# Performance work log

Measured on AMD Instinct MI355X. Metric: run time of the kernel, lower is better.

Reference implementation:

```python
import jax, jax.numpy as jnp
import numpy as np

B, C, H, W = 8, 384, 32, 32
NH, DK, DV = 8, 48, 48
CFF = 4 * C
L = H * W
NBIAS = (2 * H - 1) * (2 * W - 1)
LN_EPS = 1e-5


def _relative_indices(height, width):
    # rel_idx[q, k] = (gy_k - gy_q + H) * W + (gx_k - gx_q + W), matching the torch loop
    gy, gx = np.meshgrid(np.arange(height), np.arange(width), indexing='ij')
    gy = gy.ravel(); gx = gx.ravel()
    rel = (gy[None, :] - gy[:, None] + height) * width + (gx[None, :] - gx[:, None] + width)
    return jnp.asarray(rel, dtype=jnp.int64)


def setup_inputs() -> dict:
    key = jax.random.key(0)
    ks = jax.random.split(key, 10)
    s = 0.02  # small init scale
    return {
        'x': jax.random.normal(ks[0], (B, C, H, W), dtype=jnp.float32),
        'gamma': jnp.ones((C,), jnp.float32),
        'beta': jnp.zeros((C,), jnp.float32),
        'Wq': jax.random.normal(ks[1], (NH * DK, C), jnp.float32) * s,
        'Wk': jax.random.normal(ks[2], (NH * DK, C), jnp.float32) * s,
        'Wv': jax.random.normal(ks[3], (NH * DV, C), jnp.float32) * s,
        'Wo': jax.random.normal(ks[4], (C, NH * DV), jnp.float32) * s,
        'bo': jnp.zeros((C,), jnp.float32),
        'rel_bias': jax.random.normal(ks[5], (NH, NBIAS), jnp.float32),
        'fc1_w': jax.random.normal(ks[6], (CFF, C), jnp.float32) * s,
        'fc1_b': jnp.zeros((CFF,), jnp.float32),
        'fc2_w': jax.random.normal(ks[7], (C, CFF), jnp.float32) * s,
        'fc2_b': jnp.zeros((C,), jnp.float32),
        'rel_idx': _relative_indices(H, W),
    }


def reference(x, gamma, beta, Wq, Wk, Wv, Wo, bo, rel_bias,
              fc1_w, fc1_b, fc2_w, fc2_b, rel_idx):
    b, c, h_sp, w_sp = x.shape
    l = h_sp * w_sp
    nh = rel_bias.shape[0]
    dk = Wq.shape[0] // nh
    dv = Wv.shape[0] // nh

    # LayerNorm over channel dim (NHWC), then flatten to tokens [b, l, c]
    t = jnp.transpose(x, (0, 2, 3, 1))
    mu = jnp.mean(t, axis=-1, keepdims=True)
    var = jnp.mean(jnp.square(t - mu), axis=-1, keepdims=True)
    t = (t - mu) / jnp.sqrt(var + LN_EPS) * gamma + beta
    tok = t.reshape(b, l, c)

    q = (tok @ Wq.T).reshape(b, l, nh, dk)
    k = (tok @ Wk.T).reshape(b, l, nh, dk)
    v = (tok @ Wv.T).reshape(b, l, nh, dv)

    # gathered relative position bias: [nh, l, l]
    bias = rel_bias[:, rel_idx]
    # note: original applies NO 1/sqrt(d_k) scaling
    scores = jnp.einsum('blhd,bmhd->bhlm', q, k) + bias[None]
    attn = jax.nn.softmax(scores, axis=-1)
    out = jnp.einsum('bhlm,bmhd->blhd', attn, v).reshape(b, l, nh * dv)
    out = out @ Wo.T + bo  # [b, l, c]
    out = jnp.transpose(out, (0, 2, 1)).reshape(b, c, h_sp, w_sp)

    y = x + out  # attention residual (x_stem = x, no downsampling)

    # FFN: 1x1 convs == per-pixel linear over channels; exact (erf) gelu as torch default
    u = jnp.einsum('bchw,oc->bohw', y, fc1_w) + fc1_b[None, :, None, None]
    u = jax.nn.gelu(u, approximate=False)
    u = jnp.einsum('bchw,oc->bohw', u, fc2_w) + fc2_b[None, :, None, None]
    return y + u
```

## Files before the change

kernel.cpp:

```cpp
#include <hip/hip_runtime.h>
#include <math.h>

#define SL 1024
#define CH 384
#define NHEAD 8
#define DH 48
#define NBIAS 3969
#define NTOK 8192
#define BATCH 8
#define CFF 1536
#define LN_EPS 1e-5f
#define QKVLD 1152
#define HMS 3145728

#define WQKV_OFF 0
#define WO_OFF   442368
#define F1_OFF   589824
#define F2_OFF   1179648
#define WTOT     1769472

typedef float floatx4 __attribute__((ext_vector_type(4)));
typedef short bf16x8 __attribute__((ext_vector_type(8)));

__device__ __forceinline__ unsigned f2bf_u(float f) {
  unsigned u = __float_as_uint(f);
  return (u + 0x7fffu + ((u >> 16) & 1u)) >> 16;
}
__device__ __forceinline__ unsigned pack2(float a, float b) {
  return f2bf_u(a) | (f2bf_u(b) << 16);
}

__device__ __forceinline__ void gload_lds16(const void* g, void* l) {
  __builtin_amdgcn_global_load_lds(
      (const __attribute__((address_space(1))) void*)g,
      (__attribute__((address_space(3))) void*)l, 16, 0, 0);
}

__global__ void k_w2bf(const float* __restrict__ Wq, const float* __restrict__ Wk,
                       const float* __restrict__ Wv, const float* __restrict__ Wo,
                       const float* __restrict__ f1, const float* __restrict__ f2,
                       short* __restrict__ dst) {
  size_t i = ((size_t)blockIdx.x * 256 + threadIdx.x) * 8;
  if (i >= WTOT) return;
  const float* s;
  size_t base;
  if (i < 147456)        { s = Wq; base = 0; }
  else if (i < 294912)   { s = Wk; base = 147456; }
  else if (i < WO_OFF)   { s = Wv; base = 294912; }
  else if (i < F1_OFF)   { s = Wo; base = WO_OFF; }
  else if (i < F2_OFF)   { s = f1; base = F1_OFF; }
  else                   { s = f2; base = F2_OFF; }
  const float4* p = (const float4*)(s + (i - base));
  float4 a = p[0], b = p[1];
  uint4 o;
  o.x = pack2(a.x, a.y); o.y = pack2(a.z, a.w);
  o.z = pack2(b.x, b.y); o.w = pack2(b.z, b.w);
  *(uint4*)(dst + i) = o;
}

__global__ __launch_bounds__(256) void k_ln_fused(
    const float* __restrict__ x, const float* __restrict__ gamma,
    const float* __restrict__ beta, short* __restrict__ tok) {
  __shared__ float sx[32][385];
  int b = blockIdx.y, l0 = blockIdx.x * 32;
  int tid = threadIdx.x;
  const float* xb = x + (size_t)b * CH * SL;
  int cr = tid >> 3, ls = (tid & 7) * 4;
#pragma unroll
  for (int c0 = 0; c0 < CH; c0 += 32) {
    int c = c0 + cr;
    float4 v = *(const float4*)(xb + (size_t)c * SL + l0 + ls);
    sx[ls + 0][c] = v.x; sx[ls + 1][c] = v.y;
    sx[ls + 2][c] = v.z; sx[ls + 3][c] = v.w;
  }
  __syncthreads();
  int tl = tid >> 3, p = tid & 7;
  float vals[48];
  float s = 0.f, q = 0.f;
#pragma unroll
  for (int i = 0; i < 48; i++) {
    float v = sx[tl][p * 48 + i];
    vals[i] = v; s += v; q += v * v;
  }
  s += __shfl_xor(s, 1, 64); q += __shfl_xor(q, 1, 64);
  s += __shfl_xor(s, 2, 64); q += __shfl_xor(q, 2, 64);
  s += __shfl_xor(s, 4, 64); q += __shfl_xor(q, 4, 64);
  float mu = s * (1.0f / CH);
  float rstd = rsqrtf(q * (1.0f / CH) - mu * mu + LN_EPS);
  short* orow = tok + (size_t)(b * SL + l0 + tl) * CH + p * 48;
#pragma unroll
  for (int i = 0; i < 48; i += 2) {
    float a = (vals[i] - mu) * rstd * gamma[p * 48 + i] + beta[p * 48 + i];
    float c = (vals[i + 1] - mu) * rstd * gamma[p * 48 + i + 1] + beta[p * 48 + i + 1];
    *(unsigned*)(orow + i) = pack2(a, c);
  }
}

template <int BM, bool GELU, bool HAS_BIAS, int RES_MODE, int OUT_MODE>
__global__ __launch_bounds__(256) void k_gemm_mfma(
    const short* __restrict__ A, const short* __restrict__ W,
    const float* __restrict__ bias, const float* __restrict__ res,
    float* __restrict__ Cf, short* __restrict__ Cb, float* __restrict__ Ct,
    short* __restrict__ Chm, int N, int K) {
  constexpr int MI = BM / 32;
  constexpr int ASI = BM * 2 / 64;
  __shared__ short As[BM * 64];
  __shared__ short Bs[128 * 64];
  int tid = threadIdx.x;
  int wid = tid >> 6, lane = tid & 63;
  int lanelo = lane & 15, quad = lane >> 4;
  int wm = wid & 1, wn = wid >> 1;
  int m0 = blockIdx.y * BM, n0 = blockIdx.x * 128;

  const short* Aga[ASI];
  short* Ala[ASI];
#pragma unroll
  for (int s = 0; s < ASI; s++) {
    int p = wid * (BM * 2) + s * 64 + lane;
    int row = p >> 3, ch = (p & 7) ^ (row & 7);
    Aga[s] = A + (size_t)(m0 + row) * K + ch * 8;
    Ala[s] = As + (wid * (BM * 2) + s * 64) * 8;
  }
  const short* Bga[4];
  short* Bla[4];
#pragma unroll
  for (int s = 0; s < 4; s++) {
    int p = wid * 256 + s * 64 + lane;
    int row = p >> 3, ch = (p & 7) ^ (row & 7);
    Bga[s] = W + (size_t)(n0 + row) * K + ch * 8;
    Bla[s] = Bs + (wid * 256 + s * 64) * 8;
  }

  floatx4 acc[MI][4];
#pragma unroll
  for (int i = 0; i < MI; i++)
#pragma unroll
    for (int j = 0; j < 4; j++) acc[i][j] = {0.f, 0.f, 0.f, 0.f};

  int x8 = lanelo & 7;
  int ca0 = (quad ^ x8) * 8;
  int ca1 = ((quad + 4) ^ x8) * 8;

  for (int k0 = 0; k0 < K; k0 += 64) {
    __syncthreads();
#pragma unroll
    for (int s = 0; s < ASI; s++) gload_lds16(Aga[s] + k0, Ala[s]);
#pragma unroll
    for (int s = 0; s < 4; s++) gload_lds16(Bga[s] + k0, Bla[s]);
    __syncthreads();
#pragma unroll
    for (int h = 0; h < 2; h++) {
      int co = h ? ca1 : ca0;
      bf16x8 af[MI], bq[4];
#pragma unroll
      for (int i = 0; i < MI; i++)
        af[i] = *(const bf16x8*)&As[(wm * (BM / 2) + i * 16 + lanelo) * 64 + co];
#pragma unroll
      for (int j = 0; j < 4; j++)
        bq[j] = *(const bf16x8*)&Bs[(wn * 64 + j * 16 + lanelo) * 64 + co];
#pragma unroll
      for (int i = 0; i < MI; i++)
#pragma unroll
        for (int j = 0; j < 4; j++)
          acc[i][j] = __builtin_amdgcn_mfma_f32_16x16x32_bf16(af[i], bq[j], acc[i][j], 0, 0, 0);
    }
  }

  int colb = n0 + wn * 64 + lanelo;
  float bvv[4];
#pragma unroll
  for (int j = 0; j < 4; j++) bvv[j] = HAS_BIAS ? bias[colb + j * 16] : 0.0f;
#pragma unroll
  for (int i = 0; i < MI; i++) {
    int r = m0 + wm * (BM / 2) + i * 16 + quad * 4;
    int bb = r >> 10, ll = r & 1023;
#pragma unroll
    for (int j = 0; j < 4; j++) {
      int c = colb + j * 16;
      float4 rv = {0.f, 0.f, 0.f, 0.f};
      if (RES_MODE == 2) rv = *(const float4*)(res + ((size_t)bb * CH + c) * SL + ll);
      float vv[4];
#pragma unroll
      for (int reg = 0; reg < 4; reg++) {
        float v = acc[i][j][reg] + bvv[j];
        if (RES_MODE == 1) v += res[(size_t)(r + reg) * N + c];
        if (RES_MODE == 2) v += (&rv.x)[reg];
        if (GELU) v = 0.5f * v * (1.0f + erff(v * 0.7071067811865476f));
        vv[reg] = v;
      }
      if (OUT_MODE & 1) {
#pragma unroll
        for (int reg = 0; reg < 4; reg++) Cf[(size_t)(r + reg) * N + c] = vv[reg];
      }
      if (OUT_MODE & 2) {
#pragma unroll
        for (int reg = 0; reg < 4; reg++) Cb[(size_t)(r + reg) * N + c] = (short)f2bf_u(vv[reg]);
      }
      if (OUT_MODE & 4) {
        float4 ov = {vv[0], vv[1], vv[2], vv[3]};
        *(float4*)(Ct + ((size_t)bb * CH + c) * SL + ll) = ov;
      }
      if (OUT_MODE & 8) {
        int part = c / 384;
        int rem = c - part * 384;
        int hh = rem / 48, dd = rem - hh * 48;
        short* dst = Chm + (size_t)part * HMS +
                     ((size_t)(bb * NHEAD + hh) * SL + ll) * 48 + dd;
#pragma unroll
        for (int reg = 0; reg < 4; reg++) dst[reg * 48] = (short)f2bf_u(vv[reg]);
      }
    }
  }
}

__global__ __launch_bounds__(256) void k_attn_mfma(
    const short* __restrict__ qh, const short* __restrict__ kh,
    const short* __restrict__ vh, const float* __restrict__ rel_bias,
    short* __restrict__ ao) {
  __shared__ short QP[128 * 72];
  __shared__ short Ks[64 * 72];
  __shared__ short Vts[48 * 72];

  int b = blockIdx.z, h = blockIdx.y;
  int l0 = blockIdx.x * 128;
  int tid = threadIdx.x;
  int wid = tid >> 6, lane = tid & 63;
  int lanelo = lane & 15, quad = lane >> 4;
  size_t hb = ((size_t)b * NHEAD + h) * SL;
  size_t bSL = (size_t)b * SL;
  const float* rbh = rel_bias + h * NBIAS;
  const short* kbase = kh + hb * 48;
  const short* vbase = vh + hb * 48;

  {
    const short* qsrc = qh + (hb + l0) * 48;
    for (int g = tid; g < 768; g += 256) {
      int row = g / 6, pos = g - row * 6;
      *(uint4*)&QP[row * 72 + pos * 8] = *(const uint4*)(qsrc + g * 8);
    }
  }
  for (int z = tid; z < 128 * 8; z += 256) {
    int r = z >> 3, u = z & 7;
    ((unsigned*)&QP[r * 72 + 48])[u] = 0u;
    if (r < 64) ((unsigned*)&Ks[r * 72 + 48])[u] = 0u;
  }

  int kg = 2 * tid;
  int krow = kg / 6, kpos = kg - krow * 6;
  int vmp = tid & 31, vdg = tid >> 5;

  uint4 kr0, kr1, vr0, vr1;
  if (tid < 192) {
    kr0 = *(const uint4*)(kbase + kg * 8);
    kr1 = *(const uint4*)(kbase + kg * 8 + 8);
    const short* vs = vbase + (2 * vmp) * 48 + vdg * 8;
    vr0 = *(const uint4*)vs;
    vr1 = *(const uint4*)(vs + 48);
  }
  __syncthreads();

  bf16x8 aq[2][2];
#pragma unroll
  for (int i = 0; i < 2; i++) {
    aq[i][0] = *(const bf16x8*)&QP[(wid * 32 + i * 16 + lanelo) * 72 + quad * 8];
    aq[i][1] = *(const bf16x8*)&QP[(wid * 32 + i * 16 + lanelo) * 72 + 32 + quad * 8];
  }

  floatx4 O[2][3];
#pragma unroll
  for (int i = 0; i < 2; i++)
#pragma unroll
    for (int d = 0; d < 3; d++) O[i][d] = {0.f, 0.f, 0.f, 0.f};
  float lsum[2][4] = {{0.f, 0.f, 0.f, 0.f}, {0.f, 0.f, 0.f, 0.f}};
  int boff[2];
#pragma unroll
  for (int i = 0; i < 2; i++)
    boff[i] = 1056 - (l0 + wid * 32 + i * 16 + quad * 4) + lanelo;

  short* Pw = &QP[wid * 32 * 72];

  for (int mt = 0; mt < SL; mt += 64) {
    __syncthreads();
    if (tid < 192) {
      *(uint4*)&Ks[krow * 72 + kpos * 8] = kr0;
      *(uint4*)&Ks[krow * 72 + (kpos + 1) * 8] = kr1;
      union { uint4 u; unsigned short s[8]; } va, vb;
      va.u = vr0; vb.u = vr1;
#pragma unroll
      for (int i = 0; i < 8; i++) {
        unsigned pk = (unsigned)va.s[i] | ((unsigned)vb.s[i] << 16);
        *(unsigned*)&Vts[(vdg * 8 + i) * 72 + 2 * vmp] = pk;
      }
    }
    __syncthreads();
    if (mt + 64 < SL && tid < 192) {
      const short* ks = kbase + (size_t)(mt + 64) * 48;
      kr0 = *(const uint4*)(ks + kg * 8);
      kr1 = *(const uint4*)(ks + kg * 8 + 8);
      const short* vs = vbase + (size_t)(mt + 64 + 2 * vmp) * 48 + vdg * 8;
      vr0 = *(const uint4*)vs;
      vr1 = *(const uint4*)(vs + 48);
    }

    bf16x8 kb[4][2];
#pragma unroll
    for (int nt = 0; nt < 4; nt++) {
      kb[nt][0] = *(const bf16x8*)&Ks[(nt * 16 + lanelo) * 72 + quad * 8];
      kb[nt][1] = *(const bf16x8*)&Ks[(nt * 16 + lanelo) * 72 + 32 + quad * 8];
    }

#pragma unroll
    for (int i = 0; i < 2; i++) {
      floatx4 s[4];
#pragma unroll
      for (int nt = 0; nt < 4; nt++) {
        floatx4 a = {0.f, 0.f, 0.f, 0.f};
        a = __builtin_amdgcn_mfma_f32_16x16x32_bf16(aq[i][0], kb[nt][0], a, 0, 0, 0);
        a = __builtin_amdgcn_mfma_f32_16x16x32_bf16(aq[i][1], kb[nt][1], a, 0, 0, 0);
        s[nt] = a;
      }
#pragma unroll
      for (int nt = 0; nt < 4; nt++) {
        int mo = mt + nt * 16;
#pragma unroll
        for (int reg = 0; reg < 4; reg++) {
          float e = __expf(s[nt][reg] + rbh[boff[i] - reg + mo]);
          lsum[i][reg] += e;
          Pw[(i * 16 + quad * 4 + reg) * 72 + nt * 16 + lanelo] = (short)f2bf_u(e);
        }
      }
    }
    __asm__ volatile("s_waitcnt lgkmcnt(0)" ::: "memory");
    bf16x8 pa[2][2];
#pragma unroll
    for (int i = 0; i < 2; i++) {
      pa[i][0] = *(const bf16x8*)&Pw[(i * 16 + lanelo) * 72 + quad * 8];
      pa[i][1] = *(const bf16x8*)&Pw[(i * 16 + lanelo) * 72 + 32 + quad * 8];
    }
#pragma unroll
    for (int d = 0; d < 3; d++) {
      bf16x8 v0 = *(const bf16x8*)&Vts[(d * 16 + lanelo) * 72 + quad * 8];
      bf16x8 v1 = *(const bf16x8*)&Vts[(d * 16 + lanelo) * 72 + 32 + quad * 8];
#pragma unroll
      for (int i = 0; i < 2; i++) {
        O[i][d] = __builtin_amdgcn_mfma_f32_16x16x32_bf16(pa[i][0], v0, O[i][d], 0, 0, 0);
        O[i][d] = __builtin_amdgcn_mfma_f32_16x16x32_bf16(pa[i][1], v1, O[i][d], 0, 0, 0);
      }
    }
  }

#pragma unroll
  for (int i = 0; i < 2; i++)
#pragma unroll
    for (int reg = 0; reg < 4; reg++) {
      float s = lsum[i][reg];
      s += __shfl_xor(s, 1, 64);
      s += __shfl_xor(s, 2, 64);
      s += __shfl_xor(s, 4, 64);
      s += __shfl_xor(s, 8, 64);
      float inv = 1.0f / s;
      size_t base =
          (bSL + (size_t)(l0 + wid * 32 + i * 16 + quad * 4 + reg)) * CH + h * DH;
      ao[base + 0 + lanelo]  = (short)f2bf_u(O[i][0][reg] * inv);
      ao[base + 16 + lanelo] = (short)f2bf_u(O[i][1][reg] * inv);
      ao[base + 32 + lanelo] = (short)f2bf_u(O[i][2][reg] * inv);
    }
}

extern "C" void kernel_launch(void* const* d_in, const int* in_sizes, int n_in,
                              void* d_out, int out_size, void* d_ws, size_t ws_size,
                              hipStream_t stream) {
  const float* x = (const float*)d_in[0];
  const float* gamma = (const float*)d_in[1];
  const float* beta = (const float*)d_in[2];
  const float* Wq = (const float*)d_in[3];
  const float* Wk = (const float*)d_in[4];
  const float* Wv = (const float*)d_in[5];
  const float* Wo = (const float*)d_in[6];
  const float* bo = (const float*)d_in[7];
  const float* rel_bias = (const float*)d_in[8];
  const float* fc1_w = (const float*)d_in[9];
  const float* fc1_b = (const float*)d_in[10];
  const float* fc2_w = (const float*)d_in[11];
  const float* fc2_b = (const float*)d_in[12];
  float* out = (float*)d_out;

  const size_t TOKCH = (size_t)NTOK * CH;
  float* ws_f = (float*)d_ws;
  float* yb = ws_f;
  short* wbf    = (short*)(yb + TOKCH);
  short* tok_bf = wbf + WTOT;
  short* hm     = tok_bf + TOKCH;
  short* ao_bf  = hm + 3 * (size_t)HMS;
  short* yb_bf  = ao_bf + TOKCH;
  short* h1_bf  = yb_bf + TOKCH;

  k_w2bf<<<WTOT / 8 / 256, 256, 0, stream>>>(Wq, Wk, Wv, Wo, fc1_w, fc2_w, wbf);
  k_ln_fused<<<dim3(SL / 32, BATCH), 256, 0, stream>>>(x, gamma, beta, tok_bf);

  k_gemm_mfma<128, false, false, 0, 8>
      <<<dim3(QKVLD / 128, NTOK / 128), 256, 0, stream>>>(
          tok_bf, wbf + WQKV_OFF, nullptr, nullptr, nullptr, nullptr, nullptr,
          hm, QKVLD, CH);

  k_attn_mfma<<<dim3(SL / 128, NHEAD, BATCH), 256, 0, stream>>>(
      hm, hm + HMS, hm + 2 * (size_t)HMS, rel_bias, ao_bf);

  k_gemm_mfma<64, false, true, 2, 3>
      <<<dim3(CH / 128, NTOK / 64), 256, 0, stream>>>(
          ao_bf, wbf + WO_OFF, bo, x, yb, yb_bf, nullptr, nullptr, CH, CH);

  k_gemm_mfma<128, true, true, 0, 2>
      <<<dim3(CFF / 128, NTOK / 128), 256, 0, stream>>>(
          yb_bf, wbf + F1_OFF, fc1_b, nullptr, nullptr, h1_bf, nullptr, nullptr,
          CFF, CH);

  k_gemm_mfma<64, false, true, 1, 4>
      <<<dim3(CH / 128, NTOK / 64), 256, 0, stream>>>(
          h1_bf, wbf + F2_OFF, fc2_b, yb, nullptr, nullptr, out, nullptr, CH, CFF);
}
```

Baseline: 224.4 us.

## Stage relative-position bias slice in LDS and drop register prefetch of K/V tiles

Each attention block now copies the contiguous 1152-float window of the head's relative bias that its 128 queries need into shared memory once, and reads the bias from LDS instead of global memory inside the softmax loop. The register-based software prefetch of the next K/V tile is removed, so K/V are loaded from global directly into LDS at the start of each iteration. This aims to cut scattered global bias loads and register pressure, at the cost of exposing global K/V load latency before each tile and adding 4.5KB of LDS per block.

```diff
diff --git a/kernel.cpp b/kernel.cpp
--- a/kernel.cpp
+++ b/kernel.cpp
@@ -220,6 +220,7 @@
   __shared__ short QP[128 * 72];
   __shared__ short Ks[64 * 72];
   __shared__ short Vts[48 * 72];
+  __shared__ float Bb[1152];
 
   int b = blockIdx.z, h = blockIdx.y;
   int l0 = blockIdx.x * 128;
@@ -228,64 +229,63 @@
   int lanelo = lane & 15, quad = lane >> 4;
   size_t hb = ((size_t)b * NHEAD + h) * SL;
   size_t bSL = (size_t)b * SL;
-  const float* rbh = rel_bias + h * NBIAS;
   const short* kbase = kh + hb * 48;
   const short* vbase = vh + hb * 48;
 
   {
     const short* qsrc = qh + (hb + l0) * 48;
-    for (int g = tid; g < 768; g += 256) {
+#pragma unroll
+    for (int s = 0; s < 3; s++) {
+      int g = tid + 256 * s;
       int row = g / 6, pos = g - row * 6;
       *(uint4*)&QP[row * 72 + pos * 8] = *(const uint4*)(qsrc + g * 8);
     }
+  }
+  {
+    const float* bsrc = rel_bias + h * NBIAS + (929 - l0);
+    for (int j = tid; j < 1152; j += 256) Bb[j] = bsrc[j];
   }
   for (int z = tid; z < 128 * 8; z += 256) {
     int r = z >> 3, u = z & 7;
     ((unsigned*)&QP[r * 72 + 48])[u] = 0u;
     if (r < 64) ((unsigned*)&Ks[r * 72 + 48])[u] = 0u;
   }
+  __syncthreads();
+
+  bf16x8 aq[2][2];
+#pragma unroll
+  for (int i = 0; i < 2; i++) {
+    aq[i][0] = *(const bf16x8*)&QP[(wid * 32 + i * 16 + lanelo) * 72 + quad * 8];
+    aq[i][1] = *(const bf16x8*)&QP[(wid * 32 + i * 16 + lanelo) * 72 + 32 + quad * 8];
+  }
+
+  floatx4 O[2][3];
+#pragma unroll
+  for (int i = 0; i < 2; i++)
+#pragma unroll
+    for (int d = 0; d < 3; d++) O[i][d] = {0.f, 0.f, 0.f, 0.f};
+  float lsum[2][4] = {{0.f, 0.f, 0.f, 0.f}, {0.f, 0.f, 0.f, 0.f}};
+  int boffL[2];
+#pragma unroll
+  for (int i = 0; i < 2; i++)
+    boffL[i] = 127 - (wid * 32 + i * 16 + quad * 4) + lanelo;
 
   int kg = 2 * tid;
   int krow = kg / 6, kpos = kg - krow * 6;
   int vmp = tid & 31, vdg = tid >> 5;
 
-  uint4 kr0, kr1, vr0, vr1;
-  if (tid < 192) {
-    kr0 = *(const uint4*)(kbase + kg * 8);
-    kr1 = *(const uint4*)(kbase + kg * 8 + 8);
-    const short* vs = vbase + (2 * vmp) * 48 + vdg * 8;
-    vr0 = *(const uint4*)vs;
-    vr1 = *(const uint4*)(vs + 48);
-  }
-  __syncthreads();
-
-  bf16x8 aq[2][2];
-#pragma unroll
-  for (int i = 0; i < 2; i++) {
-    aq[i][0] = *(const bf16x8*)&QP[(wid * 32 + i * 16 + lanelo) * 72 + quad * 8];
-    aq[i][1] = *(const bf16x8*)&QP[(wid * 32 + i * 16 + lanelo) * 72 + 32 + quad * 8];
-  }
-
-  floatx4 O[2][3];
-#pragma unroll
-  for (int i = 0; i < 2; i++)
-#pragma unroll
-    for (int d = 0; d < 3; d++) O[i][d] = {0.f, 0.f, 0.f, 0.f};
-  float lsum[2][4] = {{0.f, 0.f, 0.f, 0.f}, {0.f, 0.f, 0.f, 0.f}};
-  int boff[2];
-#pragma unroll
-  for (int i = 0; i < 2; i++)
-    boff[i] = 1056 - (l0 + wid * 32 + i * 16 + quad * 4) + lanelo;
-
   short* Pw = &QP[wid * 32 * 72];
 
   for (int mt = 0; mt < SL; mt += 64) {
     __syncthreads();
     if (tid < 192) {
-      *(uint4*)&Ks[krow * 72 + kpos * 8] = kr0;
-      *(uint4*)&Ks[krow * 72 + (kpos + 1) * 8] = kr1;
+      const short* ksrc = kbase + (size_t)mt * 48 + kg * 8;
+      *(uint4*)&Ks[krow * 72 + kpos * 8] = *(const uint4*)(ksrc);
+      *(uint4*)&Ks[krow * 72 + (kpos + 1) * 8] = *(const uint4*)(ksrc + 8);
+      const short* vs = vbase + (size_t)(mt + 2 * vmp) * 48 + vdg * 8;
       union { uint4 u; unsigned short s[8]; } va, vb;
-      va.u = vr0; vb.u = vr1;
+      va.u = *(const uint4*)vs;
+      vb.u = *(const uint4*)(vs + 48);
 #pragma unroll
       for (int i = 0; i < 8; i++) {
         unsigned pk = (unsigned)va.s[i] | ((unsigned)vb.s[i] << 16);
@@ -293,14 +293,6 @@
       }
     }
     __syncthreads();
-    if (mt + 64 < SL && tid < 192) {
-      const short* ks = kbase + (size_t)(mt + 64) * 48;
-      kr0 = *(const uint4*)(ks + kg * 8);
-      kr1 = *(const uint4*)(ks + kg * 8 + 8);
-      const short* vs = vbase + (size_t)(mt + 64 + 2 * vmp) * 48 + vdg * 8;
-      vr0 = *(const uint4*)vs;
-      vr1 = *(const uint4*)(vs + 48);
-    }
 
     bf16x8 kb[4][2];
 #pragma unroll
@@ -324,7 +316,7 @@
         int mo = mt + nt * 16;
 #pragma unroll
         for (int reg = 0; reg < 4; reg++) {
-          float e = __expf(s[nt][reg] + rbh[boff[i] - reg + mo]);
+          float e = __expf(s[nt][reg] + Bb[boffL[i] - reg + mo]);
           lsum[i][reg] += e;
           Pw[(i * 16 + quad * 4 + reg) * 72 + nt * 16 + lanelo] = (short)f2bf_u(e);
         }
```

New measurement: 213.6 us. 1.05x faster.
